# Performance work log

Hardware: AMD Instinct MI355X
Metric: run time of the kernel (lower is better)

Reference implementation:

```python
import jax, jax.numpy as jnp
import numpy as np

D_MODEL = 1024
N_HEADS = 16
D_HEAD = D_MODEL // N_HEADS


def setup_inputs() -> dict:
    key = jax.random.key(0)
    ks = jax.random.split(key, 11)
    B, S = 2, 2048
    scale = 1.0 / np.sqrt(D_MODEL)
    inp = {
        "query": jax.random.normal(ks[0], (B, S, D_MODEL), jnp.float32),
        "key": jax.random.normal(ks[1], (B, S, D_MODEL), jnp.float32),
        "value": jax.random.normal(ks[2], (B, S, D_MODEL), jnp.float32),
        "Wq": jax.random.normal(ks[3], (D_MODEL, D_MODEL), jnp.float32) * scale,
        "bq": jnp.zeros((D_MODEL,), jnp.float32),
        "Wk": jax.random.normal(ks[4], (D_MODEL, D_MODEL), jnp.float32) * scale,
        "bk": jnp.zeros((D_MODEL,), jnp.float32),
        "Wv": jax.random.normal(ks[5], (D_MODEL, D_MODEL), jnp.float32) * scale,
        "bv": jnp.zeros((D_MODEL,), jnp.float32),
        "Wo": jax.random.normal(ks[6], (D_MODEL, D_MODEL), jnp.float32) * scale,
        "bo": jnp.zeros((D_MODEL,), jnp.float32),
    }
    return inp


def _split_heads(x):
    B, S, _ = x.shape
    return x.reshape(B, S, N_HEADS, D_HEAD).transpose(0, 2, 1, 3)  # [B,H,S,Dh]


def reference(query, key, value, Wq, bq, Wk, bk, Wv, bv, Wo, bo):
    q = _split_heads(query @ Wq + bq)
    k = _split_heads(key @ Wk + bk)
    v = _split_heads(value @ Wv + bv)
    # scores [B,H,S,S] -- faithfully materialized as in the original
    scores = jnp.einsum("bhqd,bhkd->bhqk", q, k) / np.sqrt(D_HEAD)
    attn = jax.nn.softmax(scores, axis=-1)
    out = jnp.einsum("bhqk,bhkd->bhqd", attn, v)  # [B,H,S,Dh]
    B, H, S, Dh = out.shape
    out = out.transpose(0, 2, 1, 3).reshape(B, S, H * Dh)
    return out @ Wo + bo
```

## Files before the change

kernel.cpp:

```cpp
#include <hip/hip_runtime.h>
#include <hip/hip_bf16.h>

using bf16 = __hip_bfloat16;
typedef __bf16 bf16x8 __attribute__((ext_vector_type(8)));
typedef __bf16 bf16x2v __attribute__((ext_vector_type(2)));
typedef float f32x4 __attribute__((ext_vector_type(4)));
typedef float f32x16 __attribute__((ext_vector_type(16)));

#define SEQ 2048
#define DM  1024
#define QSCALE 0.18033688011112042f

__device__ __forceinline__ f32x4 mfma16(bf16x8 a, bf16x8 b, f32x4 c) {
  return __builtin_amdgcn_mfma_f32_16x16x32_bf16(a, b, c, 0, 0, 0);
}
__device__ __forceinline__ f32x16 mfma32(bf16x8 a, bf16x8 b, f32x16 c) {
  return __builtin_amdgcn_mfma_f32_32x32x16_bf16(a, b, c, 0, 0, 0);
}
__device__ __forceinline__ void gload16(const void* g, void* l) {
  __builtin_amdgcn_global_load_lds(
      (const __attribute__((address_space(1))) unsigned int*)g,
      (__attribute__((address_space(3))) unsigned int*)l, 16, 0, 0);
}
__device__ __forceinline__ unsigned short bfbits(float x) {
  bf16 h = __float2bfloat16(x);
  return *reinterpret_cast<unsigned short*>(&h);
}
__device__ __forceinline__ unsigned pk2(float a, float b) {
#if __has_builtin(__builtin_amdgcn_cvt_pk_bf16_f32)
  bf16x2v r = __builtin_amdgcn_cvt_pk_bf16_f32(a, b);
  return *reinterpret_cast<unsigned*>(&r);
#else
  return (unsigned)bfbits(a) | ((unsigned)bfbits(b) << 16);
#endif
}
__device__ __forceinline__ float fexp2(float x) {
#if __has_builtin(__builtin_amdgcn_exp2f)
  return __builtin_amdgcn_exp2f(x);
#else
  return exp2f(x);
#endif
}
__device__ __forceinline__ void plswap(unsigned& a, unsigned& b) {
  asm("v_permlane32_swap_b32 %0, %1" : "+v"(a), "+v"(b));
}

__global__ __launch_bounds__(256) void cast_all(const float* __restrict__ q,
                                                const float* __restrict__ k,
                                                const float* __restrict__ v,
                                                const float* __restrict__ Wq,
                                                const float* __restrict__ Wk,
                                                const float* __restrict__ Wv,
                                                const float* __restrict__ Wo,
                                                bf16* __restrict__ Lx,
                                                bf16* __restrict__ Lw,
                                                bf16* __restrict__ Lwo) {
  __shared__ float tf[64][68];
  if (blockIdx.y < 3) {
    const float* src = blockIdx.y == 0 ? q : (blockIdx.y == 1 ? k : v);
    bf16* dst = Lx + (size_t)blockIdx.y * (4096ull * 1024) + (size_t)blockIdx.x * 16384;
#pragma unroll
    for (int i = 0; i < 8; ++i) {
      int u = threadIdx.x + i * 256;
      int k32 = u >> 6, l = u & 63;
      const float* p = src + (size_t)(blockIdx.x * 16 + (l & 15)) * 1024 + k32 * 32 + (l >> 4) * 8;
      float4 a = *(const float4*)p;
      float4 b = *(const float4*)(p + 4);
      alignas(16) unsigned o[4] = {pk2(a.x, a.y), pk2(a.z, a.w), pk2(b.x, b.y), pk2(b.z, b.w)};
      *(uint4*)(dst + (size_t)u * 8) = *(const uint4*)o;
    }
    return;
  }
  const int widx = blockIdx.y - 3;
  const float* W = widx == 0 ? Wq : (widx == 1 ? Wk : (widx == 2 ? Wv : Wo));
  bf16* dst = widx < 3 ? (Lw + (size_t)widx * 1048576) : Lwo;
  const int t = threadIdx.x, bx = blockIdx.x & 15, by = blockIdx.x >> 4;
#pragma unroll
  for (int i = 0; i < 4; ++i) {
    int u = t + i * 256, r = u >> 4, c4 = u & 15;
    *(float4*)&tf[r][c4 * 4] = *(const float4*)(W + (size_t)(by * 64 + r) * 1024 + bx * 64 + c4 * 4);
  }
  __syncthreads();
#pragma unroll
  for (int i = 0; i < 2; ++i) {
    int u = t + i * 256;
    int sub = u >> 6, l = u & 63;
    int n16l = sub >> 1, k32l = sub & 1;
    int nn = n16l * 16 + (l & 15);
    int kk = k32l * 32 + (l >> 4) * 8;
    alignas(16) unsigned o[4];
#pragma unroll
    for (int p = 0; p < 4; ++p) o[p] = pk2(tf[kk + 2 * p][nn], tf[kk + 2 * p + 1][nn]);
    size_t off = ((((size_t)(bx * 4 + n16l)) * 32 + (by * 2 + k32l)) * 64 + l) * 8;
    *(uint4*)(dst + off) = *(const uint4*)o;
  }
}

__global__ __launch_bounds__(512, 2) void qkv_gemm(const bf16* __restrict__ Lw,
                                                   const bf16* __restrict__ Lx,
                                                   const float* __restrict__ bq,
                                                   const float* __restrict__ bk,
                                                   const float* __restrict__ bv,
                                                   bf16* __restrict__ Lq,
                                                   bf16* __restrict__ Lk,
                                                   bf16* __restrict__ Lv) {
  __shared__ alignas(16) bf16 At[2][16384];
  __shared__ alignas(16) bf16 Bt[2][16384];
  const int t = threadIdx.x, lane = t & 63, w = t >> 6;
  const int m16 = lane & 15, g4 = lane >> 4;
  const int bid = blockIdx.y * 16 + blockIdx.x;
  const int logical = (bid & 7) * 24 + (bid >> 3);
  const int nt = logical & 15, ym = logical >> 4;
  const int third = ym >> 2, mt = ym & 3;
  const int wm = w >> 2, wn = w & 3;
  const bf16* Wb = Lw + (size_t)third * 1048576;
  const bf16* Xb = Lx + (size_t)third * (4096ull * 1024);
  f32x4 acc[8][4] = {};

#pragma unroll
  for (int ii = 0; ii < 4; ++ii) {
    int u = w * 4 + ii;
    gload16(Wb + (((size_t)(mt * 16 + (u >> 1)) * 32 + (u & 1)) * 64 + lane) * 8, (void*)&At[0][u * 512]);
    gload16(Xb + (((size_t)(nt * 16 + (u >> 1)) * 32 + (u & 1)) * 64 + lane) * 8, (void*)&Bt[0][u * 512]);
  }
  __syncthreads();

  const bf16* Ab0 = (third < 2) ? At[0] : Bt[0];
  const bf16* Bb0 = (third < 2) ? Bt[0] : At[0];

  int cur = 0;
  for (int slab = 0; slab < 16; ++slab) {
    if (slab < 15) {
      const int nb = cur ^ 1, k2 = (slab + 1) * 2;
#pragma unroll
      for (int ii = 0; ii < 4; ++ii) {
        int u = w * 4 + ii;
        gload16(Wb + (((size_t)(mt * 16 + (u >> 1)) * 32 + k2 + (u & 1)) * 64 + lane) * 8,
                (void*)&At[nb][u * 512]);
        gload16(Xb + (((size_t)(nt * 16 + (u >> 1)) * 32 + k2 + (u & 1)) * 64 + lane) * 8,
                (void*)&Bt[nb][u * 512]);
      }
    }
    const bf16* Ac = Ab0 + cur * 16384;
    const bf16* Bc = Bb0 + cur * 16384;
#pragma unroll
    for (int kc = 0; kc < 2; ++kc) {
      bf16x8 bfr[4];
#pragma unroll
      for (int nj = 0; nj < 4; ++nj)
        bfr[nj] = *(const bf16x8*)&Bc[((wn * 4 + nj) * 2 + kc) * 512 + lane * 8];
#pragma unroll
      for (int mh = 0; mh < 2; ++mh) {
        bf16x8 afr[4];
#pragma unroll
        for (int i = 0; i < 4; ++i)
          afr[i] = *(const bf16x8*)&Ac[((wm * 8 + mh * 4 + i) * 2 + kc) * 512 + lane * 8];
        __builtin_amdgcn_s_setprio(1);
#pragma unroll
        for (int i = 0; i < 4; ++i)
#pragma unroll
          for (int nj = 0; nj < 4; ++nj)
            acc[mh * 4 + i][nj] = mfma16(afr[i], bfr[nj], acc[mh * 4 + i][nj]);
        __builtin_amdgcn_s_setprio(0);
      }
    }
    __syncthreads();
    cur ^= 1;
  }

  if (third < 2) {
    bf16* dst = third == 0 ? Lq : Lk;
    const float* bias = third == 0 ? bq : bk;
    const float sc = third == 0 ? QSCALE : 1.0f;
#pragma unroll
    for (int mi = 0; mi < 8; ++mi) {
      int doutb = mt * 256 + wm * 128 + mi * 16 + g4 * 4;
      float4 b4 = *(const float4*)(bias + doutb);
      int hh = doutb >> 6, d32 = (doutb & 63) >> 5;
      int lhi = (doutb & 31) >> 3, half = g4 & 1;
#pragma unroll
      for (int nj = 0; nj < 4; ++nj) {
        int seq = nt * 256 + wn * 64 + nj * 16 + m16;
        int bb2 = seq >> 11, s16w = (seq & 2047) >> 4;
        size_t off = ((((size_t)(bb2 * 128 + s16w)) * 16 + hh) * 2 + d32) * 512 + (m16 + 16 * lhi) * 8 + half * 4;
        uint2 pv;
        pv.x = pk2((acc[mi][nj][0] + b4.x) * sc, (acc[mi][nj][1] + b4.y) * sc);
        pv.y = pk2((acc[mi][nj][2] + b4.z) * sc, (acc[mi][nj][3] + b4.w) * sc);
        *(uint2*)(dst + off) = pv;
      }
    }
  } else {
#pragma unroll
    for (int nj = 0; nj < 4; ++nj) {
      int dout = mt * 256 + wn * 64 + nj * 16 + m16;
      float bvv = bv[dout];
      int hh = dout >> 6, dt = (dout & 63) >> 4;
#pragma unroll
      for (int mi = 0; mi < 8; ++mi) {
        int seqb = nt * 256 + wm * 128 + mi * 16 + g4 * 4;
        int b_ = seqb >> 11, kt = (seqb & 2047) >> 6, ks32 = (seqb & 63) >> 5;
        int lhi = (seqb & 31) >> 3, half = g4 & 1;
        size_t off = (((((size_t)(b_ * 32 + kt)) * 16 + hh) * 4 + dt) * 2 + ks32) * 512 + (m16 + 16 * lhi) * 8 + half * 4;
        uint2 pv;
        pv.x = pk2(acc[mi][nj][0] + bvv, acc[mi][nj][1] + bvv);
        pv.y = pk2(acc[mi][nj][2] + bvv, acc[mi][nj][3] + bvv);
        *(uint2*)(Lv + off) = pv;
      }
    }
  }
}

__global__ __launch_bounds__(512, 4) void flash(const bf16* __restrict__ Lq,
                                                const bf16* __restrict__ Lk,
                                                const bf16* __restrict__ Lv,
                                                bf16* __restrict__ Lab) {
  __shared__ alignas(16) unsigned char smem[65536];
  bf16* const Kb = (bf16*)smem;
  bf16* const Vb = (bf16*)(smem + 32768);

  const int t = threadIdx.x, lane = t & 63, w = t >> 6;
  const int l31 = lane & 31, m16 = lane & 15, hi = lane >> 5, b4 = (lane >> 4) & 1;
  const int qw = w >> 1, g = w & 1, wg = w >> 1;
  const int bid = blockIdx.x;
  const int logical = ((bid & 7) << 6) | (bid >> 3);
  const int qt = logical & 15, h = (logical >> 4) & 15, b = logical >> 8;

  bf16x8 qf[4];
  {
    const int sQ = b * 128 + qt * 8 + qw * 2 + b4;
#pragma unroll
    for (int ks = 0; ks < 4; ++ks) {
      const int d32 = ks >> 1, g4q = (ks & 1) * 2 + hi;
      qf[ks] = *(const bf16x8*)(Lq + (((size_t)sQ * 16 + h) * 2 + d32) * 512 + (m16 + 16 * g4q) * 8);
    }
  }

  const int ss = wg >> 1, sd = wg & 1;
#pragma unroll
  for (int u = 0; u < 2; ++u) {
    const bf16* gk = Lk + ((((size_t)(b * 128 + g * 64 + u * 2 + ss)) * 16 + h) * 2 + sd) * 512 + lane * 8;
    gload16(gk, (void*)(Kb + (g * 2 + 0) * 4096 + u * 2048 + wg * 512));
    const bf16* gv = Lv + (((((size_t)(b * 32 + g * 16)) * 16 + h) * 4 + wg) * 2 + u) * 512 + lane * 8;
    gload16(gv, (void*)(Vb + (g * 2 + 0) * 4096 + u * 2048 + wg * 512));
  }

  float lrow = 0.f;
  f32x16 oacc[2] = {};
  __syncthreads();

  for (int it = 0; it < 16; ++it) {
    const int cur = it & 1;
    const bf16* const Klb = Kb + (g * 2 + cur) * 4096;
    const bf16* const Vlb = Vb + (g * 2 + cur) * 4096;
    if (it < 15) {
      const int nb = cur ^ 1;
#pragma unroll
      for (int u = 0; u < 2; ++u) {
        const int kc = (it + 1) * 2 + u;
        const bf16* gk = Lk + ((((size_t)(b * 128 + g * 64 + kc * 2 + ss)) * 16 + h) * 2 + sd) * 512 + lane * 8;
        gload16(gk, (void*)(Kb + (g * 2 + nb) * 4096 + u * 2048 + wg * 512));
        const bf16* gv = Lv + (((((size_t)(b * 32 + g * 16 + (kc >> 1))) * 16 + h) * 4 + wg) * 2 + (kc & 1)) * 512 + lane * 8;
        gload16(gv, (void*)(Vb + (g * 2 + nb) * 4096 + u * 2048 + wg * 512));
      }
    }

#pragma unroll
    for (int u = 0; u < 2; ++u) {
      const bf16* const Kl = Klb + u * 2048;
      const bf16* const Vl = Vlb + u * 2048;

      f32x16 s = {};
      __builtin_amdgcn_s_setprio(1);
#pragma unroll
      for (int ks = 0; ks < 4; ++ks) {
        const int d32 = ks >> 1, g4k = (ks & 1) * 2 + hi;
        bf16x8 kf = *(const bf16x8*)&Kl[((b4 * 2 + d32) * 64 + m16 + 16 * g4k) * 8];
        s = mfma32(kf, qf[ks], s);
      }
      __builtin_amdgcn_s_setprio(0);

      float e[16];
#pragma unroll
      for (int r = 0; r < 16; ++r) e[r] = fexp2(s[r]);
      {
        float a0 = e[0] + e[1], a1 = e[2] + e[3], a2 = e[4] + e[5], a3 = e[6] + e[7];
        float a4 = e[8] + e[9], a5 = e[10] + e[11], a6 = e[12] + e[13], a7 = e[14] + e[15];
        lrow += ((a0 + a1) + (a2 + a3)) + ((a4 + a5) + (a6 + a7));
      }
      bf16x8 bP[2];
#pragma unroll
      for (int c = 0; c < 2; ++c) {
        unsigned P0 = pk2(e[8 * c + 0], e[8 * c + 1]);
        unsigned P1 = pk2(e[8 * c + 2], e[8 * c + 3]);
        unsigned P2 = pk2(e[8 * c + 4], e[8 * c + 5]);
        unsigned P3 = pk2(e[8 * c + 6], e[8 * c + 7]);
        plswap(P0, P2);
        plswap(P1, P3);
        alignas(16) unsigned pw[4] = {P0, P1, P2, P3};
        bP[c] = *(const bf16x8*)pw;
      }

      __builtin_amdgcn_s_setprio(1);
#pragma unroll
      for (int dtile = 0; dtile < 2; ++dtile) {
        const int dt = dtile * 2 + b4;
#pragma unroll
        for (int c = 0; c < 2; ++c) {
          bf16x8 av = *(const bf16x8*)&Vl[(dt * 64 + m16 + 16 * (2 * c + hi)) * 8];
          oacc[dtile] = mfma32(av, bP[c], oacc[dtile]);
        }
      }
      __builtin_amdgcn_s_setprio(0);
    }
    __syncthreads();
  }

  lrow += __shfl_xor(lrow, 32);

  float* const Os = (float*)smem;
  float* const Ls = (float*)(smem + 32768);
  if (g == 1) {
#pragma unroll
    for (int dtile = 0; dtile < 2; ++dtile)
#pragma unroll
      for (int r = 0; r < 16; ++r)
        Os[((qw * 2 + dtile) * 16 + r) * 64 + lane] = oacc[dtile][r];
    if (hi == 0) Ls[qw * 32 + l31] = lrow;
  }
  __syncthreads();
  if (g == 0) {
    const float inv = 1.f / (lrow + Ls[qw * 32 + l31]);
    const int sQ = b * 128 + qt * 8 + qw * 2 + b4;
#pragma unroll
    for (int dtile = 0; dtile < 2; ++dtile) {
      const int k32 = h * 2 + dtile;
#pragma unroll
      for (int j = 0; j < 8; ++j) {
        const int r = 2 * j;
        float o0 = oacc[dtile][r] + Os[((qw * 2 + dtile) * 16 + r) * 64 + lane];
        float o1 = oacc[dtile][r + 1] + Os[((qw * 2 + dtile) * 16 + r + 1) * 64 + lane];
        unsigned pv = pk2(o0 * inv, o1 * inv);
        size_t off = ((size_t)sQ * 32 + k32) * 512 + (m16 + 16 * (r >> 2)) * 8 + 4 * hi + (r & 3);
        *(unsigned*)(Lab + off) = pv;
      }
    }
  }
}

__global__ __launch_bounds__(256) void out_gemm(const bf16* __restrict__ Lab,
                                                const bf16* __restrict__ Lwo,
                                                const float* __restrict__ bo,
                                                float* __restrict__ out) {
  __shared__ alignas(16) bf16 Al[8192];
  __shared__ alignas(16) bf16 Bl[4096];
  const int t = threadIdx.x, lane = t & 63, w = t >> 6;
  const int m16 = lane & 15, g4 = lane >> 4;
  const int nt = blockIdx.x, mt = blockIdx.y;
  const int wm = w >> 1, wn = w & 1;
  f32x4 acc[4][2] = {};

  for (int slab = 0; slab < 16; ++slab) {
#pragma unroll
    for (int ii = 0; ii < 4; ++ii) {
      int s = w * 4 + ii;
      const bf16* gp = Lab + (((size_t)(mt * 8 + (s >> 1))) * 32 + slab * 2 + (s & 1)) * 512 + lane * 8;
      gload16(gp, (void*)&Al[s * 512]);
    }
#pragma unroll
    for (int ii = 0; ii < 2; ++ii) {
      int s = w * 2 + ii;
      const bf16* gp = Lwo + (((size_t)(nt * 4 + (s >> 1))) * 32 + slab * 2 + (s & 1)) * 512 + lane * 8;
      gload16(gp, (void*)&Bl[s * 512]);
    }
    __syncthreads();
#pragma unroll
    for (int c = 0; c < 2; ++c) {
      bf16x8 aA[4], bW[2];
#pragma unroll
      for (int i = 0; i < 4; ++i) aA[i] = *(const bf16x8*)&Al[((wm * 4 + i) * 2 + c) * 512 + lane * 8];
#pragma unroll
      for (int j = 0; j < 2; ++j) bW[j] = *(const bf16x8*)&Bl[((wn * 2 + j) * 2 + c) * 512 + lane * 8];
#pragma unroll
      for (int i = 0; i < 4; ++i)
#pragma unroll
        for (int j = 0; j < 2; ++j) acc[i][j] = mfma16(aA[i], bW[j], acc[i][j]);
    }
    __syncthreads();
  }
#pragma unroll
  for (int j = 0; j < 2; ++j) {
    int n = nt * 64 + wn * 32 + j * 16 + m16;
    float bb = bo[n];
#pragma unroll
    for (int i = 0; i < 4; ++i) {
      int seqb = mt * 128 + wm * 64 + i * 16 + g4 * 4;
#pragma unroll
      for (int r = 0; r < 4; ++r) out[(size_t)(seqb + r) * 1024 + n] = acc[i][j][r] + bb;
    }
  }
}

extern "C" void kernel_launch(void* const* d_in, const int* in_sizes, int n_in,
                              void* d_out, int out_size, void* d_ws, size_t ws_size,
                              hipStream_t stream) {
  const float* query = (const float*)d_in[0];
  const float* key   = (const float*)d_in[1];
  const float* value = (const float*)d_in[2];
  const float* Wq = (const float*)d_in[3];
  const float* bq = (const float*)d_in[4];
  const float* Wk = (const float*)d_in[5];
  const float* bk = (const float*)d_in[6];
  const float* Wv = (const float*)d_in[7];
  const float* bv = (const float*)d_in[8];
  const float* Wo = (const float*)d_in[9];
  const float* bo = (const float*)d_in[10];
  float* out = (float*)d_out;

  bf16* Lw  = (bf16*)d_ws;
  bf16* Lwo = Lw + 3ull * 1048576;
  bf16* Lx  = Lwo + 1048576;
  bf16* Lq  = Lx + 3ull * 4194304;
  bf16* Lk  = Lq + 4194304;
  bf16* Lv  = Lk + 4194304;
  bf16* Lab = Lv + 4194304;

  cast_all<<<dim3(256, 7), 256, 0, stream>>>(query, key, value, Wq, Wk, Wv, Wo, Lx, Lw, Lwo);
  qkv_gemm<<<dim3(16, 12), 512, 0, stream>>>(Lw, Lx, bq, bk, bv, Lq, Lk, Lv);
  flash<<<512, 512, 0, stream>>>(Lq, Lk, Lv, Lab);
  out_gemm<<<dim3(16, 32), 256, 0, stream>>>(Lab, Lwo, bo, out);
}
```

Before: 215.1 us.

## Double-buffer output GEMM and relax QKV GEMM waits to partial vmcnt

In the QKV projection GEMM, the full __syncthreads at the end of each slab is replaced by a raw s_barrier plus a partial vmcnt wait, so the next slab's loads can stay in flight while the current slab computes. The output GEMM gets double-buffered LDS, a prologue prefetch, the same partial-wait barrier scheme, MFMA priority hints and a remapped block order for L2 locality. This aims to hide global-to-LDS latency behind compute. The cost is twice the LDS in the output GEMM and a dependence on hand-counted vmcnt values being correct.

```diff
diff --git a/kernel.cpp b/kernel.cpp
--- a/kernel.cpp
+++ b/kernel.cpp
@@ -123,13 +123,14 @@
     gload16(Wb + (((size_t)(mt * 16 + (u >> 1)) * 32 + (u & 1)) * 64 + lane) * 8, (void*)&At[0][u * 512]);
     gload16(Xb + (((size_t)(nt * 16 + (u >> 1)) * 32 + (u & 1)) * 64 + lane) * 8, (void*)&Bt[0][u * 512]);
   }
-  __syncthreads();
 
   const bf16* Ab0 = (third < 2) ? At[0] : Bt[0];
   const bf16* Bb0 = (third < 2) ? Bt[0] : At[0];
 
   int cur = 0;
   for (int slab = 0; slab < 16; ++slab) {
+    __builtin_amdgcn_s_barrier();
+    __builtin_amdgcn_sched_barrier(0);
     if (slab < 15) {
       const int nb = cur ^ 1, k2 = (slab + 1) * 2;
 #pragma unroll
@@ -140,7 +141,14 @@
         gload16(Xb + (((size_t)(nt * 16 + (u >> 1)) * 32 + k2 + (u & 1)) * 64 + lane) * 8,
                 (void*)&Bt[nb][u * 512]);
       }
-    }
+      asm volatile("s_waitcnt vmcnt(8)" ::: "memory");
+    } else {
+      asm volatile("s_waitcnt vmcnt(0)" ::: "memory");
+    }
+    __builtin_amdgcn_sched_barrier(0);
+    __builtin_amdgcn_s_barrier();
+    __builtin_amdgcn_sched_barrier(0);
+
     const bf16* Ac = Ab0 + cur * 16384;
     const bf16* Bc = Bb0 + cur * 16384;
 #pragma unroll
@@ -164,7 +172,6 @@
         __builtin_amdgcn_s_setprio(0);
       }
     }
-    __syncthreads();
     cur ^= 1;
   }
 
@@ -351,41 +358,67 @@
                                                 const bf16* __restrict__ Lwo,
                                                 const float* __restrict__ bo,
                                                 float* __restrict__ out) {
-  __shared__ alignas(16) bf16 Al[8192];
-  __shared__ alignas(16) bf16 Bl[4096];
+  __shared__ alignas(16) bf16 Al[2][8192];
+  __shared__ alignas(16) bf16 Bl[2][4096];
   const int t = threadIdx.x, lane = t & 63, w = t >> 6;
   const int m16 = lane & 15, g4 = lane >> 4;
-  const int nt = blockIdx.x, mt = blockIdx.y;
+  const int bid = blockIdx.y * 16 + blockIdx.x;
+  const int logical = (bid & 7) * 64 + (bid >> 3);
+  const int nt = logical & 15, mt = logical >> 4;
   const int wm = w >> 1, wn = w & 1;
   f32x4 acc[4][2] = {};
 
+#pragma unroll
+  for (int ii = 0; ii < 4; ++ii) {
+    int s = w * 4 + ii;
+    gload16(Lab + (((size_t)(mt * 8 + (s >> 1))) * 32 + (s & 1)) * 512 + lane * 8, (void*)&Al[0][s * 512]);
+  }
+#pragma unroll
+  for (int ii = 0; ii < 2; ++ii) {
+    int s = w * 2 + ii;
+    gload16(Lwo + (((size_t)(nt * 4 + (s >> 1))) * 32 + (s & 1)) * 512 + lane * 8, (void*)&Bl[0][s * 512]);
+  }
+
+  int cur = 0;
   for (int slab = 0; slab < 16; ++slab) {
-#pragma unroll
-    for (int ii = 0; ii < 4; ++ii) {
-      int s = w * 4 + ii;
-      const bf16* gp = Lab + (((size_t)(mt * 8 + (s >> 1))) * 32 + slab * 2 + (s & 1)) * 512 + lane * 8;
-      gload16(gp, (void*)&Al[s * 512]);
-    }
-#pragma unroll
-    for (int ii = 0; ii < 2; ++ii) {
-      int s = w * 2 + ii;
-      const bf16* gp = Lwo + (((size_t)(nt * 4 + (s >> 1))) * 32 + slab * 2 + (s & 1)) * 512 + lane * 8;
-      gload16(gp, (void*)&Bl[s * 512]);
-    }
-    __syncthreads();
+    __builtin_amdgcn_s_barrier();
+    __builtin_amdgcn_sched_barrier(0);
+    if (slab < 15) {
+      const int nb = cur ^ 1, ns = slab + 1;
+#pragma unroll
+      for (int ii = 0; ii < 4; ++ii) {
+        int s = w * 4 + ii;
+        gload16(Lab + (((size_t)(mt * 8 + (s >> 1))) * 32 + ns * 2 + (s & 1)) * 512 + lane * 8,
+                (void*)&Al[nb][s * 512]);
+      }
+#pragma unroll
+      for (int ii = 0; ii < 2; ++ii) {
+        int s = w * 2 + ii;
+        gload16(Lwo + (((size_t)(nt * 4 + (s >> 1))) * 32 + ns * 2 + (s & 1)) * 512 + lane * 8,
+                (void*)&Bl[nb][s * 512]);
+      }
+      asm volatile("s_waitcnt vmcnt(6)" ::: "memory");
+    } else {
+      asm volatile("s_waitcnt vmcnt(0)" ::: "memory");
+    }
+    __builtin_amdgcn_sched_barrier(0);
+    __builtin_amdgcn_s_barrier();
+    __builtin_amdgcn_sched_barrier(0);
 #pragma unroll
     for (int c = 0; c < 2; ++c) {
       bf16x8 aA[4], bW[2];
 #pragma unroll
-      for (int i = 0; i < 4; ++i) aA[i] = *(const bf16x8*)&Al[((wm * 4 + i) * 2 + c) * 512 + lane * 8];
-#pragma unroll
-      for (int j = 0; j < 2; ++j) bW[j] = *(const bf16x8*)&Bl[((wn * 2 + j) * 2 + c) * 512 + lane * 8];
+      for (int i = 0; i < 4; ++i) aA[i] = *(const bf16x8*)&Al[cur][((wm * 4 + i) * 2 + c) * 512 + lane * 8];
+#pragma unroll
+      for (int j = 0; j < 2; ++j) bW[j] = *(const bf16x8*)&Bl[cur][((wn * 2 + j) * 2 + c) * 512 + lane * 8];
+      __builtin_amdgcn_s_setprio(1);
 #pragma unroll
       for (int i = 0; i < 4; ++i)
 #pragma unroll
         for (int j = 0; j < 2; ++j) acc[i][j] = mfma16(aA[i], bW[j], acc[i][j]);
-    }
-    __syncthreads();
+      __builtin_amdgcn_s_setprio(0);
+    }
+    cur ^= 1;
   }
 #pragma unroll
   for (int j = 0; j < 2; ++j) {
```

Result: no change. 215.8 us (+0.3%).
